# Performance work log

Measured on AMD Instinct MI355X. Metric: run time of the kernel, lower is better.

The kernel has to match this reference:

```python
import jax, jax.numpy as jnp
import numpy as np

N, E, T, F, HID, NCLS = 50000, 800000, 6, 64, 48, 2
LN_EPS = 1e-5


def setup_inputs() -> dict:
    key = jax.random.key(0)
    ks = jax.random.split(key, 24)
    p = lambda k, shape, s=0.1: jax.random.normal(k, shape, dtype=jnp.float32) * s
    inp = {
        "x_seq": jax.random.normal(ks[0], (T, N, F), dtype=jnp.float32),
        "edge_index": jax.random.randint(ks[1], (2, E), 0, N, dtype=jnp.int64),
        "edge_weight": jax.random.uniform(ks[2], (E,), dtype=jnp.float32),
        # GCN layer 0
        "W0": p(ks[3], (F, HID)), "b0": jnp.zeros((HID,), jnp.float32),
        "g0": jnp.ones((HID,), jnp.float32), "be0": jnp.zeros((HID,), jnp.float32),
        # GCN layer 1
        "W1": p(ks[4], (HID, HID)), "b1": jnp.zeros((HID,), jnp.float32),
        "g1": jnp.ones((HID,), jnp.float32), "be1": jnp.zeros((HID,), jnp.float32),
        # GRU (torch gate order: r, z, n)
        "W_ih": p(ks[5], (3 * HID, HID)), "W_hh": p(ks[6], (3 * HID, HID)),
        "b_ih": jnp.zeros((3 * HID,), jnp.float32), "b_hh": jnp.zeros((3 * HID,), jnp.float32),
        # classifier MLP
        "Wc1": p(ks[7], (HID, HID // 2)), "bc1": jnp.zeros((HID // 2,), jnp.float32),
        "Wc2": p(ks[8], (HID // 2, NCLS)), "bc2": jnp.zeros((NCLS,), jnp.float32),
    }
    return inp


def _layer_norm(x, g, b):
    mu = x.mean(-1, keepdims=True)
    var = ((x - mu) ** 2).mean(-1, keepdims=True)
    return (x - mu) * jax.lax.rsqrt(var + LN_EPS) * g + b


def reference(x_seq, edge_index, edge_weight, W0, b0, g0, be0, W1, b1, g1, be1,
              W_ih, W_hh, b_ih, b_hh, Wc1, bc1, Wc2, bc2):
    n = x_seq.shape[1]
    hid = W0.shape[1]
    row, col = edge_index[0], edge_index[1]
    # PyG GCNConv default: add self-loops (weight 1), symmetric normalization
    loop = jnp.arange(n)
    row_f = jnp.concatenate([row, loop])
    col_f = jnp.concatenate([col, loop])
    w_f = jnp.concatenate([edge_weight, jnp.ones((n,), edge_weight.dtype)])
    deg = jax.ops.segment_sum(w_f, col_f, num_segments=n)
    dis = jnp.where(deg > 0, jax.lax.rsqrt(jnp.maximum(deg, 1e-12)), 0.0)
    norm = dis[row_f] * w_f * dis[col_f]  # [E+N]

    def gcn(x, W, b):
        h = x @ W                              # [N, hid]
        msg = h[row_f] * norm[:, None]         # [E+N, hid]
        return jax.ops.segment_sum(msg, col_f, num_segments=n) + b

    def spatial(x_t):
        # layer 0: no residual (in_dim != hid)
        h1 = jax.nn.relu(_layer_norm(gcn(x_t, W0, b0), g0, be0))
        # layer 1: residual (dropout is eval-mode no-op)
        h2 = jax.nn.relu(_layer_norm(gcn(h1, W1, b1), g1, be1)) + h1
        return h2

    # sequential map over T keeps per-step [E,hid] message buffers small
    H = jax.lax.map(spatial, x_seq)            # [T, N, hid]

    def gru_step(h, x_t):
        gi = x_t @ W_ih.T + b_ih               # [N, 3*hid]
        gh = h @ W_hh.T + b_hh
        i_r, i_z, i_n = jnp.split(gi, 3, axis=-1)
        h_r, h_z, h_n = jnp.split(gh, 3, axis=-1)
        r = jax.nn.sigmoid(i_r + h_r)
        z = jax.nn.sigmoid(i_z + h_z)
        nv = jnp.tanh(i_n + r * h_n)
        h_new = (1.0 - z) * nv + z * h
        return h_new, None

    h0 = jnp.zeros((n, hid), x_seq.dtype)
    z_last, _ = jax.lax.scan(gru_step, h0, H)  # last hidden state [N, hid]

    logits = jax.nn.relu(z_last @ Wc1 + bc1) @ Wc2 + bc2  # [N, 2]
    return logits
```

## Files before the change

kernel.cpp:

```cpp
#include <hip/hip_runtime.h>
#include <hip/hip_fp16.h>
#include <math.h>

#define NN 50000
#define NE 800000
#define TT 6
#define HID 48
#define NB 196
#define LR 65

__device__ __forceinline__ float sigmoidf_(float x){ return 1.0f/(1.0f+__expf(-x)); }
__device__ __forceinline__ float tanhf_(float x){
  float xc = fminf(fmaxf(x,-15.f),15.f);
  float t = __expf(2.f*xc);
  return (t-1.f)/(t+1.f);
}
__device__ __forceinline__ unsigned f2bf(float x){
  unsigned u = __float_as_uint(x);
  return (u + 0x7fffu + ((u>>16)&1u)) >> 16;
}
__device__ __forceinline__ unsigned pack2(float a, float b){
  return f2bf(a) | (f2bf(b)<<16);
}
__device__ __forceinline__ float bflo(unsigned u){ return __uint_as_float(u<<16); }
__device__ __forceinline__ float bfhi(unsigned u){ return __uint_as_float(u & 0xffff0000u); }
__device__ __forceinline__ unsigned f2h(float x){
  return (unsigned)__half_as_ushort(__float2half(x));
}
__device__ __forceinline__ float h2f(unsigned u){
  return __half2float(__ushort_as_half((unsigned short)(u & 0xffffu)));
}
__device__ __forceinline__ unsigned pack2h(float a, float b){
  return f2h(a) | (f2h(b)<<16);
}

typedef __fp16 h2t __attribute__((ext_vector_type(2)));

__device__ __forceinline__ unsigned pkrtz(float a, float b){
#if __has_builtin(__builtin_amdgcn_cvt_pkrtz)
  auto r = __builtin_amdgcn_cvt_pkrtz(a, b);
  return __builtin_bit_cast(unsigned, r);
#else
  return pack2h(a, b);
#endif
}
__device__ __forceinline__ float dot2f(unsigned a, unsigned b, float c){
#if __has_builtin(__builtin_amdgcn_fdot2)
  return __builtin_amdgcn_fdot2(__builtin_bit_cast(h2t, a), __builtin_bit_cast(h2t, b), c, false);
#else
  h2t av = __builtin_bit_cast(h2t, a), bv = __builtin_bit_cast(h2t, b);
  return c + (float)av[0]*(float)bv[0] + (float)av[1]*(float)bv[1];
#endif
}

struct U3 { unsigned x,y,z; };

__device__ __forceinline__ int block_scan_incl(int x, int* wsum){
  int lane = threadIdx.x & 63, w = threadIdx.x >> 6;
  int v = x;
#pragma unroll
  for(int d=1; d<64; d<<=1){
    int u = __shfl_up(v, d, 64);
    if(lane >= d) v += u;
  }
  if(lane==63) wsum[w] = v;
  __syncthreads();
  int add = 0;
#pragma unroll
  for(int k=0;k<3;k++) if(w>k) add += wsum[k];
  return v + add;
}

__global__ __launch_bounds__(256) void k_setup(int* cnt,
                                               const float* __restrict__ Wih, const float* __restrict__ Whh,
                                               unsigned* Wxp, unsigned* Whp){
  int i = blockIdx.x*256+threadIdx.x;
  if(i<NN) cnt[i]=0;
  if(i < 24*144){
    int k2 = i/144, gf = i%144;
    Wxp[i] = pack2h(Wih[gf*48 + 2*k2], Wih[gf*48 + 2*k2 + 1]);
  }
  if(i < 6*24*24){
    int wv = i/576, r = i%576;
    int k2 = r/24, c = r%24;
    int row = (c<8) ? (wv*8 + c) : (c<16) ? (48 + wv*8 + c-8) : (96 + wv*8 + c-16);
    Whp[i] = pack2h(Whh[row*48 + 2*k2], Whh[row*48 + 2*k2 + 1]);
  }
}

__global__ __launch_bounds__(256) void k_cnt(const int* __restrict__ ei, int* cnt, int* pos){
  int e = blockIdx.x*256+threadIdx.x;
  if(e<NE){
    int c = ei[NE+e];
    pos[e] = atomicAdd(&cnt[c], 1);
  }
}

__global__ __launch_bounds__(256) void k_partA(const int* __restrict__ cnt, int* bsum){
  __shared__ int wsum[4];
  int i = blockIdx.x*256+threadIdx.x;
  int x = (i<NN)? cnt[i] : 0;
  int lane = threadIdx.x & 63, w = threadIdx.x >> 6;
  int v = x;
#pragma unroll
  for(int m=32;m>=1;m>>=1) v += __shfl_xor(v, m, 64);
  if(lane==0) wsum[w]=v;
  __syncthreads();
  if(threadIdx.x==0) bsum[blockIdx.x] = wsum[0]+wsum[1]+wsum[2]+wsum[3];
}

__global__ __launch_bounds__(256) void k_midB(const int* __restrict__ bsum, int* bpre, int* offs){
  __shared__ int wsum[4];
  int t = threadIdx.x;
  int x = (t<NB)? bsum[t] : 0;
  int incl = block_scan_incl(x, wsum);
  if(t<NB) bpre[t] = incl - x;
  if(t==255) offs[NN] = incl;
}

__global__ __launch_bounds__(256) void k_offsC(const int* __restrict__ cnt, const int* __restrict__ bpre,
                                               int* offs){
  __shared__ int wsum[4];
  int i = blockIdx.x*256+threadIdx.x;
  int x = (i<NN)? cnt[i] : 0;
  int incl = block_scan_incl(x, wsum);
  if(i<NN) offs[i] = bpre[blockIdx.x] + incl - x;
}

__global__ __launch_bounds__(256) void k_scatter(const int* __restrict__ ei, const float* __restrict__ ew,
                                                 const int* __restrict__ offs, const int* __restrict__ pos,
                                                 int2* __restrict__ csr){
  int e = blockIdx.x*256+threadIdx.x;
  if(e<NE){
    int c = ei[NE+e];
    int2 v; v.x = ei[e]; v.y = __float_as_int(ew[e]);
    csr[offs[c]+pos[e]] = v;
  }
}

__global__ __launch_bounds__(256) void k_deg(const int2* __restrict__ csr, const int* __restrict__ offs,
                                             float* dis){
  int i = blockIdx.x*256+threadIdx.x;
  if(i<NN){
    float s = 1.f;
    int e0=offs[i], e1=offs[i+1];
    for(int j=e0;j<e1;j++) s += __int_as_float(csr[j].y);
    dis[i] = rsqrtf(s);
  }
}

__global__ __launch_bounds__(256) void k_normE(int2* __restrict__ csr, const float* __restrict__ dis){
  int j = blockIdx.x*256+threadIdx.x;
  if(j<NE){
    int2 v = csr[j];
    v.y = __float_as_int(dis[v.x]*__int_as_float(v.y));
    csr[j] = v;
  }
}

__global__ __launch_bounds__(256) void k_mm0(const float* __restrict__ X, const float* __restrict__ W,
                                             unsigned* __restrict__ A){
  int s = __builtin_amdgcn_readfirstlane(threadIdx.x>>6);
  int n = blockIdx.x*64 + (threadIdx.x&63);
  if(n>=NN) return;
  const float* xb = X + (long long)n*64;
  const float* wb = W + 12*s;
  float acc[TT][12];
#pragma unroll
  for(int t=0;t<TT;t++)
#pragma unroll
    for(int j=0;j<12;j++) acc[t][j]=0.f;
#pragma unroll 2
  for(int k4=0;k4<16;k4++){
    float4 xv[TT];
#pragma unroll
    for(int t=0;t<TT;t++) xv[t] = *reinterpret_cast<const float4*>(xb + (long long)t*NN*64 + 4*k4);
#pragma unroll
    for(int q=0;q<4;q++){
      const float* wr = wb + (4*k4+q)*HID;
      float w[12];
#pragma unroll
      for(int j=0;j<12;j++) w[j]=wr[j];
#pragma unroll
      for(int t=0;t<TT;t++){
        float xs = (&xv[t].x)[q];
#pragma unroll
        for(int j=0;j<12;j++) acc[t][j] = fmaf(xs, w[j], acc[t][j]);
      }
    }
  }
  unsigned buf[36];
#pragma unroll
  for(int j=0;j<12;j++){
    buf[3*j  ]=pack2(acc[0][j],acc[1][j]);
    buf[3*j+1]=pack2(acc[2][j],acc[3][j]);
    buf[3*j+2]=pack2(acc[4][j],acc[5][j]);
  }
  uint4* o4 = reinterpret_cast<uint4*>(A + (long long)n*144 + 36*s);
#pragma unroll
  for(int q=0;q<9;q++) o4[q] = make_uint4(buf[4*q],buf[4*q+1],buf[4*q+2],buf[4*q+3]);
}

__global__ __launch_bounds__(256) void k_mm1(const float* __restrict__ X, const float* __restrict__ W,
                                             unsigned* __restrict__ A){
  int s = __builtin_amdgcn_readfirstlane(threadIdx.x>>6);
  int n = blockIdx.x*64 + (threadIdx.x&63);
  if(n>=NN) return;
  const float* xb = X + (long long)n*(TT*HID);
  const float* wb = W + 12*s;
  float acc[TT][12];
#pragma unroll
  for(int t=0;t<TT;t++)
#pragma unroll
    for(int j=0;j<12;j++) acc[t][j]=0.f;
#pragma unroll 2
  for(int k4=0;k4<12;k4++){
    float4 xv[TT];
#pragma unroll
    for(int t=0;t<TT;t++) xv[t] = *reinterpret_cast<const float4*>(xb + t*HID + 4*k4);
#pragma unroll
    for(int q=0;q<4;q++){
      const float* wr = wb + (4*k4+q)*HID;
      float w[12];
#pragma unroll
      for(int j=0;j<12;j++) w[j]=wr[j];
#pragma unroll
      for(int t=0;t<TT;t++){
        float xs = (&xv[t].x)[q];
#pragma unroll
        for(int j=0;j<12;j++) acc[t][j] = fmaf(xs, w[j], acc[t][j]);
      }
    }
  }
  unsigned buf[36];
#pragma unroll
  for(int j=0;j<12;j++){
    buf[3*j  ]=pack2(acc[0][j],acc[1][j]);
    buf[3*j+1]=pack2(acc[2][j],acc[3][j]);
    buf[3*j+2]=pack2(acc[4][j],acc[5][j]);
  }
  uint4* o4 = reinterpret_cast<uint4*>(A + (long long)n*144 + 36*s);
#pragma unroll
  for(int q=0;q<9;q++) o4[q] = make_uint4(buf[4*q],buf[4*q+1],buf[4*q+2],buf[4*q+3]);
}

__global__ __launch_bounds__(256) void k_agg(const unsigned* __restrict__ A, const float* __restrict__ bias,
                                             const float* __restrict__ gain, const float* __restrict__ beta,
                                             const float* __restrict__ resid, float* __restrict__ out,
                                             const int* __restrict__ offs, const int2* __restrict__ csr,
                                             const float* __restrict__ dis){
  int wid = (blockIdx.x*256+threadIdx.x)>>6;
  int lane = threadIdx.x & 63;
  if(wid>=NN) return;
  const bool act = lane<HID;
  const int f = act? lane : (HID-1);
  float dn = dis[wid];
  float acc[TT];
  {
    U3 v = *reinterpret_cast<const U3*>(A + (long long)wid*144 + 3*f);
    acc[0]=dn*bflo(v.x); acc[1]=dn*bfhi(v.x);
    acc[2]=dn*bflo(v.y); acc[3]=dn*bfhi(v.y);
    acc[4]=dn*bflo(v.z); acc[5]=dn*bfhi(v.z);
  }
  int e0=offs[wid], e1=offs[wid+1];
  int e=e0;
  for(; e+3<e1; e+=4){
    int2 i0=csr[e], i1=csr[e+1], i2=csr[e+2], i3=csr[e+3];
    U3 d0 = *reinterpret_cast<const U3*>(A + (long long)i0.x*144 + 3*f);
    U3 d1 = *reinterpret_cast<const U3*>(A + (long long)i1.x*144 + 3*f);
    U3 d2 = *reinterpret_cast<const U3*>(A + (long long)i2.x*144 + 3*f);
    U3 d3 = *reinterpret_cast<const U3*>(A + (long long)i3.x*144 + 3*f);
    float n0=__int_as_float(i0.y), n1=__int_as_float(i1.y);
    float n2=__int_as_float(i2.y), n3=__int_as_float(i3.y);
    acc[0]=fmaf(n0,bflo(d0.x),acc[0]); acc[1]=fmaf(n0,bfhi(d0.x),acc[1]);
    acc[2]=fmaf(n0,bflo(d0.y),acc[2]); acc[3]=fmaf(n0,bfhi(d0.y),acc[3]);
    acc[4]=fmaf(n0,bflo(d0.z),acc[4]); acc[5]=fmaf(n0,bfhi(d0.z),acc[5]);
    acc[0]=fmaf(n1,bflo(d1.x),acc[0]); acc[1]=fmaf(n1,bfhi(d1.x),acc[1]);
    acc[2]=fmaf(n1,bflo(d1.y),acc[2]); acc[3]=fmaf(n1,bfhi(d1.y),acc[3]);
    acc[4]=fmaf(n1,bflo(d1.z),acc[4]); acc[5]=fmaf(n1,bfhi(d1.z),acc[5]);
    acc[0]=fmaf(n2,bflo(d2.x),acc[0]); acc[1]=fmaf(n2,bfhi(d2.x),acc[1]);
    acc[2]=fmaf(n2,bflo(d2.y),acc[2]); acc[3]=fmaf(n2,bfhi(d2.y),acc[3]);
    acc[4]=fmaf(n2,bflo(d2.z),acc[4]); acc[5]=fmaf(n2,bfhi(d2.z),acc[5]);
    acc[0]=fmaf(n3,bflo(d3.x),acc[0]); acc[1]=fmaf(n3,bfhi(d3.x),acc[1]);
    acc[2]=fmaf(n3,bflo(d3.y),acc[2]); acc[3]=fmaf(n3,bfhi(d3.y),acc[3]);
    acc[4]=fmaf(n3,bflo(d3.z),acc[4]); acc[5]=fmaf(n3,bfhi(d3.z),acc[5]);
  }
  for(; e<e1; ++e){
    int2 i0=csr[e];
    U3 d0 = *reinterpret_cast<const U3*>(A + (long long)i0.x*144 + 3*f);
    float n0=__int_as_float(i0.y);
    acc[0]=fmaf(n0,bflo(d0.x),acc[0]); acc[1]=fmaf(n0,bfhi(d0.x),acc[1]);
    acc[2]=fmaf(n0,bflo(d0.y),acc[2]); acc[3]=fmaf(n0,bfhi(d0.y),acc[3]);
    acc[4]=fmaf(n0,bflo(d0.z),acc[4]); acc[5]=fmaf(n0,bfhi(d0.z),acc[5]);
  }
  float bb = bias[f], gg = gain[f], be = beta[f];
  const float rn = 1.0f/HID;
#pragma unroll
  for(int t=0;t<TT;t++){
    float val = fmaf(acc[t], dn, bb);
    float v = act? val : 0.f;
    float s = v, s2 = v*v;
#pragma unroll
    for(int m=32;m>=1;m>>=1){
      s  += __shfl_xor(s,  m, 64);
      s2 += __shfl_xor(s2, m, 64);
    }
    float mu  = s*rn;
    float var = fmaxf(s2*rn - mu*mu, 0.f);
    float y = (val-mu)*rsqrtf(var+1e-5f)*gg + be;
    y = fmaxf(y, 0.f);
    long long oidx = (long long)wid*(TT*HID) + t*HID + f;
    if(resid) y += resid[oidx];
    if(act) out[oidx] = y;
  }
}

__global__ __launch_bounds__(384) void k_gi(const float* __restrict__ X,
                                            const unsigned* __restrict__ Wxp,
                                            const float* __restrict__ bih,
                                            unsigned* __restrict__ gi){
  int wv = __builtin_amdgcn_readfirstlane(threadIdx.x>>6);
  int lane = threadIdx.x & 63;
  long long n = (long long)blockIdx.x*64 + lane;
  long long gn = (n < NN)? n : (NN-1);
  const bool wr = (n < NN);
  const float* xb = X + gn*(TT*HID) + wv*HID;
  unsigned xp[24];
#pragma unroll
  for(int q=0;q<12;q++){
    float4 v = *reinterpret_cast<const float4*>(xb + 4*q);
    xp[2*q]   = pkrtz(v.x, v.y);
    xp[2*q+1] = pkrtz(v.z, v.w);
  }
#pragma unroll 1
  for(int pass=0; pass<3; pass++){
    float acc[48];
#pragma unroll
    for(int j=0;j<48;j++) acc[j] = bih[pass*48+j];
#pragma unroll 2
    for(int k2=0;k2<24;k2++){
      unsigned xk = xp[k2];
#pragma unroll
      for(int c=0;c<2;c++){
        const unsigned* wp = Wxp + k2*144 + pass*48 + c*24;
        unsigned ws[24];
#pragma unroll
        for(int j=0;j<24;j++) ws[j]=wp[j];
#pragma unroll
        for(int j=0;j<24;j++) acc[c*24+j] = dot2f(xk, ws[j], acc[c*24+j]);
      }
    }
    if(wr){
      unsigned* ob = gi + ((long long)(wv*72 + pass*24))*NN + n;
#pragma unroll
      for(int m=0;m<24;m++){
        ob[(long long)m*NN] = pack2h(acc[2*m], acc[2*m+1]);
      }
    }
  }
}

__global__ __launch_bounds__(384) void k_gruH(const unsigned* __restrict__ gi,
                                              const unsigned* __restrict__ Whp,
                                              const float* __restrict__ bhh,
                                              const float* __restrict__ Wc1, const float* __restrict__ bc1,
                                              const float* __restrict__ Wc2, const float* __restrict__ bc2,
                                              float* __restrict__ out){
  __shared__ unsigned hb[2][24*64];
  int tid = threadIdx.x;
  int wv = __builtin_amdgcn_readfirstlane(tid>>6);
  int lane = tid & 63;
  int f0 = wv*8;
  long long n = (long long)blockIdx.x*64 + lane;
  long long gn = (n<NN)? n : (NN-1);

  for(int i=tid;i<24*64;i+=384) hb[0][i]=0u;

  float rb[8], zb[8], nb[8], hprev[8];
#pragma unroll
  for(int j=0;j<8;j++){
    rb[j]=bhh[f0+j]; zb[j]=bhh[48+f0+j]; nb[j]=bhh[96+f0+j];
    hprev[j]=0.f;
  }
  __syncthreads();

  int cur=0;
  for(int t=0;t<TT;t++){
    const unsigned* gb = gi + (long long)t*72*NN + gn;
    unsigned gpk[12];
#pragma unroll
    for(int m=0;m<4;m++){
      gpk[m]   = gb[(long long)(      wv*4+m)*NN];
      gpk[4+m] = gb[(long long)(24 +  wv*4+m)*NN];
      gpk[8+m] = gb[(long long)(48 +  wv*4+m)*NN];
    }
    float acc[24];
#pragma unroll
    for(int j=0;j<24;j++) acc[j]=0.f;
    const unsigned* hbc = &hb[cur][0];
#pragma unroll 2
    for(int k2=0;k2<24;k2++){
      const unsigned* wp = Whp + (wv*24+k2)*24;
      unsigned ws[24];
#pragma unroll
      for(int q=0;q<24;q++) ws[q]=wp[q];
      unsigned h2k = hbc[k2*64+lane];
#pragma unroll
      for(int c=0;c<24;c++) acc[c] = dot2f(h2k, ws[c], acc[c]);
    }
    unsigned* hw = &hb[cur^1][0];
    float hn[8];
#pragma unroll
    for(int j=0;j<8;j++){
      unsigned pr=gpk[j>>1], pz=gpk[4+(j>>1)], pn=gpk[8+(j>>1)];
      float gir = (j&1)? h2f(pr>>16) : h2f(pr);
      float giz = (j&1)? h2f(pz>>16) : h2f(pz);
      float gin = (j&1)? h2f(pn>>16) : h2f(pn);
      float r  = sigmoidf_(acc[j]+rb[j]+gir);
      float zg = sigmoidf_(acc[8+j]+zb[j]+giz);
      float ng = tanhf_(gin + r*(acc[16+j]+nb[j]));
      float hv = (1.f-zg)*ng + zg*hprev[j];
      hprev[j]=hv; hn[j]=hv;
    }
#pragma unroll
    for(int m=0;m<4;m++) hw[(wv*4+m)*64+lane] = pack2h(hn[2*m], hn[2*m+1]);
    __syncthreads();
    cur^=1;
  }

  if(wv==0 && n<NN){
    const unsigned* hbc=&hb[cur][0];
    float hv[24];
#pragma unroll
    for(int j=0;j<24;j++) hv[j]=bc1[j];
    for(int k2=0;k2<24;k2++){
      unsigned u = hbc[k2*64+lane];
      float hk0 = h2f(u), hk1 = h2f(u>>16);
      const float* w0 = Wc1 + (2*k2)*24;
      const float* w1 = Wc1 + (2*k2+1)*24;
#pragma unroll
      for(int j=0;j<24;j++) hv[j] = fmaf(hk0, w0[j], hv[j]);
#pragma unroll
      for(int j=0;j<24;j++) hv[j] = fmaf(hk1, w1[j], hv[j]);
    }
    float l0=bc2[0], l1=bc2[1];
#pragma unroll
    for(int j=0;j<24;j++){
      float a = fmaxf(hv[j],0.f);
      l0 = fmaf(a, Wc2[2*j],   l0);
      l1 = fmaf(a, Wc2[2*j+1], l1);
    }
    reinterpret_cast<float2*>(out)[n] = make_float2(l0,l1);
  }
}

static inline size_t al256(size_t x){ return (x+255)&~(size_t)255; }

extern "C" void kernel_launch(void* const* d_in, const int* in_sizes, int n_in,
                              void* d_out, int out_size, void* d_ws, size_t ws_size,
                              hipStream_t stream){
  const float* x_seq=(const float*)d_in[0];
  const int*   ei   =(const int*)d_in[1];
  const float* ew   =(const float*)d_in[2];
  const float* W0=(const float*)d_in[3];  const float* b0=(const float*)d_in[4];
  const float* g0=(const float*)d_in[5];  const float* be0=(const float*)d_in[6];
  const float* W1=(const float*)d_in[7];  const float* b1=(const float*)d_in[8];
  const float* g1=(const float*)d_in[9];  const float* be1=(const float*)d_in[10];
  const float* Wih=(const float*)d_in[11];const float* Whh=(const float*)d_in[12];
  const float* bih=(const float*)d_in[13];const float* bhh=(const float*)d_in[14];
  const float* Wc1=(const float*)d_in[15];const float* bc1=(const float*)d_in[16];
  const float* Wc2=(const float*)d_in[17];const float* bc2=(const float*)d_in[18];
  float* outp=(float*)d_out;

  char* p=(char*)d_ws; size_t off=0;
  auto alloc=[&](size_t bytes)->void*{ void* r=p+off; off=al256(off+bytes); return r; };
  float* dis    =(float*)alloc((size_t)NN*4);
  int*   cnt    =(int*)  alloc((size_t)NN*4);
  int*   offs   =(int*)  alloc((size_t)(NN+1)*4);
  int*   bsum   =(int*)  alloc((size_t)NB*4);
  int*   bpre   =(int*)  alloc((size_t)NB*4);
  int*   pos    =(int*)  alloc((size_t)NE*4);
  int2*  csr    =(int2*) alloc((size_t)NE*8);
  unsigned* Wxp =(unsigned*)alloc((size_t)24*144*4);
  unsigned* Whp =(unsigned*)alloc((size_t)6*24*24*4);
  unsigned* A   =(unsigned*)alloc((size_t)NN*576 + 1024);
  float* h1     =(float*)alloc((size_t)NN*TT*HID*4);
  float* h2     =(float*)alloc((size_t)NN*TT*HID*4);
  unsigned* gi  =(unsigned*)A;

  const int GN=(NN+255)/256, GE=(NE+255)/256;
  const int GMM=(NN+63)/64;
  const int GAGG=(NN*64+255)/256;
  const int GGRU=(NN+63)/64;

  k_setup  <<<GN,256,0,stream>>>(cnt,Wih,Whh,Wxp,Whp);
  k_cnt    <<<GE,256,0,stream>>>(ei,cnt,pos);
  k_partA  <<<NB,256,0,stream>>>(cnt,bsum);
  k_midB   <<<1,256,0,stream>>>(bsum,bpre,offs);
  k_offsC  <<<NB,256,0,stream>>>(cnt,bpre,offs);
  k_scatter<<<GE,256,0,stream>>>(ei,ew,offs,pos,csr);
  k_deg    <<<GN,256,0,stream>>>(csr,offs,dis);
  k_normE  <<<GE,256,0,stream>>>(csr,dis);

  k_mm0<<<GMM,256,0,stream>>>(x_seq, W0, A);
  k_agg<<<GAGG,256,0,stream>>>(A,b0,g0,be0,nullptr,h1,offs,csr,dis);
  k_mm1<<<GMM,256,0,stream>>>(h1, W1, A);
  k_agg<<<GAGG,256,0,stream>>>(A,b1,g1,be1,h1,h2,offs,csr,dis);
  k_gi  <<<GMM,384,0,stream>>>(h2, Wxp, bih, gi);
  k_gruH<<<GGRU,384,0,stream>>>(gi, Whp, bhh, Wc1,bc1,Wc2,bc2, outp);
}
```

Before: 699.6 us.

## Store GRU hidden state node-major in LDS and pad recurrent weight rows

The GRU kernel's shared hidden-state buffer becomes node-major with a padded stride of 28 words. Each lane now reads its whole 48-wide hidden vector with six 128-bit LDS loads into registers and writes its 8 outputs with one 128-bit store, instead of doing per-k scalar LDS reads. Recurrent weight rows are padded to 32 words so scalar loads are aligned, and the hidden bias is folded into the accumulator init. Loops in the input-projection and classifier kernels are fully unrolled, which adds register pressure.

```diff
diff --git a/kernel.cpp b/kernel.cpp
--- a/kernel.cpp
+++ b/kernel.cpp
@@ -7,7 +7,7 @@
 #define TT 6
 #define HID 48
 #define NB 196
-#define LR 65
+#define HS 28
 
 __device__ __forceinline__ float sigmoidf_(float x){ return 1.0f/(1.0f+__expf(-x)); }
 __device__ __forceinline__ float tanhf_(float x){
@@ -84,7 +84,7 @@
     int wv = i/576, r = i%576;
     int k2 = r/24, c = r%24;
     int row = (c<8) ? (wv*8 + c) : (c<16) ? (48 + wv*8 + c-8) : (96 + wv*8 + c-16);
-    Whp[i] = pack2h(Whh[row*48 + 2*k2], Whh[row*48 + 2*k2 + 1]);
+    Whp[(wv*24+k2)*32 + c] = pack2h(Whh[row*48 + 2*k2], Whh[row*48 + 2*k2 + 1]);
   }
 }
 
@@ -337,7 +337,7 @@
     float acc[48];
 #pragma unroll
     for(int j=0;j<48;j++) acc[j] = bih[pass*48+j];
-#pragma unroll 2
+#pragma unroll
     for(int k2=0;k2<24;k2++){
       unsigned xk = xp[k2];
 #pragma unroll
@@ -366,7 +366,7 @@
                                               const float* __restrict__ Wc1, const float* __restrict__ bc1,
                                               const float* __restrict__ Wc2, const float* __restrict__ bc2,
                                               float* __restrict__ out){
-  __shared__ unsigned hb[2][24*64];
+  __shared__ __align__(16) unsigned hb[2][64*HS];
   int tid = threadIdx.x;
   int wv = __builtin_amdgcn_readfirstlane(tid>>6);
   int lane = tid & 63;
@@ -374,7 +374,7 @@
   long long n = (long long)blockIdx.x*64 + lane;
   long long gn = (n<NN)? n : (NN-1);
 
-  for(int i=tid;i<24*64;i+=384) hb[0][i]=0u;
+  for(int i=tid;i<64*HS;i+=384) hb[0][i]=0u;
 
   float rb[8], zb[8], nb[8], hprev[8];
 #pragma unroll
@@ -394,21 +394,27 @@
       gpk[4+m] = gb[(long long)(24 +  wv*4+m)*NN];
       gpk[8+m] = gb[(long long)(48 +  wv*4+m)*NN];
     }
+    unsigned hreg[24];
+    {
+      const uint4* hr4 = reinterpret_cast<const uint4*>(&hb[cur][lane*HS]);
+#pragma unroll
+      for(int q=0;q<6;q++){
+        uint4 v = hr4[q];
+        hreg[4*q]=v.x; hreg[4*q+1]=v.y; hreg[4*q+2]=v.z; hreg[4*q+3]=v.w;
+      }
+    }
     float acc[24];
 #pragma unroll
-    for(int j=0;j<24;j++) acc[j]=0.f;
-    const unsigned* hbc = &hb[cur][0];
-#pragma unroll 2
+    for(int j=0;j<8;j++){ acc[j]=rb[j]; acc[8+j]=zb[j]; acc[16+j]=nb[j]; }
+#pragma unroll
     for(int k2=0;k2<24;k2++){
-      const unsigned* wp = Whp + (wv*24+k2)*24;
+      const unsigned* wp = Whp + (wv*24+k2)*32;
       unsigned ws[24];
 #pragma unroll
       for(int q=0;q<24;q++) ws[q]=wp[q];
-      unsigned h2k = hbc[k2*64+lane];
-#pragma unroll
-      for(int c=0;c<24;c++) acc[c] = dot2f(h2k, ws[c], acc[c]);
-    }
-    unsigned* hw = &hb[cur^1][0];
+#pragma unroll
+      for(int c=0;c<24;c++) acc[c] = dot2f(hreg[k2], ws[c], acc[c]);
+    }
     float hn[8];
 #pragma unroll
     for(int j=0;j<8;j++){
@@ -416,26 +422,35 @@
       float gir = (j&1)? h2f(pr>>16) : h2f(pr);
       float giz = (j&1)? h2f(pz>>16) : h2f(pz);
       float gin = (j&1)? h2f(pn>>16) : h2f(pn);
-      float r  = sigmoidf_(acc[j]+rb[j]+gir);
-      float zg = sigmoidf_(acc[8+j]+zb[j]+giz);
-      float ng = tanhf_(gin + r*(acc[16+j]+nb[j]));
+      float r  = sigmoidf_(acc[j]+gir);
+      float zg = sigmoidf_(acc[8+j]+giz);
+      float ng = tanhf_(gin + r*acc[16+j]);
       float hv = (1.f-zg)*ng + zg*hprev[j];
       hprev[j]=hv; hn[j]=hv;
     }
-#pragma unroll
-    for(int m=0;m<4;m++) hw[(wv*4+m)*64+lane] = pack2h(hn[2*m], hn[2*m+1]);
+    *reinterpret_cast<uint4*>(&hb[cur^1][lane*HS + wv*4]) =
+        make_uint4(pack2h(hn[0],hn[1]), pack2h(hn[2],hn[3]),
+                   pack2h(hn[4],hn[5]), pack2h(hn[6],hn[7]));
     __syncthreads();
     cur^=1;
   }
 
   if(wv==0 && n<NN){
-    const unsigned* hbc=&hb[cur][0];
+    unsigned hh[24];
+    {
+      const uint4* hr4 = reinterpret_cast<const uint4*>(&hb[cur][lane*HS]);
+#pragma unroll
+      for(int q=0;q<6;q++){
+        uint4 v = hr4[q];
+        hh[4*q]=v.x; hh[4*q+1]=v.y; hh[4*q+2]=v.z; hh[4*q+3]=v.w;
+      }
+    }
     float hv[24];
 #pragma unroll
     for(int j=0;j<24;j++) hv[j]=bc1[j];
+#pragma unroll
     for(int k2=0;k2<24;k2++){
-      unsigned u = hbc[k2*64+lane];
-      float hk0 = h2f(u), hk1 = h2f(u>>16);
+      float hk0 = h2f(hh[k2]), hk1 = h2f(hh[k2]>>16);
       const float* w0 = Wc1 + (2*k2)*24;
       const float* w1 = Wc1 + (2*k2+1)*24;
 #pragma unroll
@@ -482,7 +497,7 @@
   int*   pos    =(int*)  alloc((size_t)NE*4);
   int2*  csr    =(int2*) alloc((size_t)NE*8);
   unsigned* Wxp =(unsigned*)alloc((size_t)24*144*4);
-  unsigned* Whp =(unsigned*)alloc((size_t)6*24*24*4);
+  unsigned* Whp =(unsigned*)alloc((size_t)6*24*32*4);
   unsigned* A   =(unsigned*)alloc((size_t)NN*576 + 1024);
   float* h1     =(float*)alloc((size_t)NN*TT*HID*4);
   float* h2     =(float*)alloc((size_t)NN*TT*HID*4);
```

Measured after the change: 923.5 us. +32.0%, slower.

## Fuse GRU input projection into recurrent kernel, staging inputs in LDS

Applied to the files above, without the earlier changes.

Removes the separate k_gi kernel, which wrote fp16 gate pre-activations for all timesteps to global memory, and computes the input projection inside the recurrent GRU kernel. Each block stages its nodes' six timesteps of h2 into shared memory as packed fp16, then each timestep does combined dot2 accumulation over the hidden and input weights from one interleaved weight array. Input and hidden biases are folded into the accumulator initialisation. This drops a large global write and re-read of the gi buffer and one launch, at the cost of more shared memory per block (about 49KB) and more registers in the recurrent loop, which may lower occupancy.

```diff
diff --git a/kernel.cpp b/kernel.cpp
--- a/kernel.cpp
+++ b/kernel.cpp
@@ -7,7 +7,6 @@
 #define TT 6
 #define HID 48
 #define NB 196
-#define LR 65
 
 __device__ __forceinline__ float sigmoidf_(float x){ return 1.0f/(1.0f+__expf(-x)); }
 __device__ __forceinline__ float tanhf_(float x){
@@ -73,18 +72,16 @@
 
 __global__ __launch_bounds__(256) void k_setup(int* cnt,
                                                const float* __restrict__ Wih, const float* __restrict__ Whh,
-                                               unsigned* Wxp, unsigned* Whp){
+                                               unsigned* Wall){
   int i = blockIdx.x*256+threadIdx.x;
   if(i<NN) cnt[i]=0;
-  if(i < 24*144){
-    int k2 = i/144, gf = i%144;
-    Wxp[i] = pack2h(Wih[gf*48 + 2*k2], Wih[gf*48 + 2*k2 + 1]);
-  }
-  if(i < 6*24*24){
-    int wv = i/576, r = i%576;
-    int k2 = r/24, c = r%24;
-    int row = (c<8) ? (wv*8 + c) : (c<16) ? (48 + wv*8 + c-8) : (96 + wv*8 + c-16);
-    Whp[i] = pack2h(Whh[row*48 + 2*k2], Whh[row*48 + 2*k2 + 1]);
+  if(i < 6*24*48){
+    int wv = i/1152, r = i%1152;
+    int k2 = r/48, c = r%48;
+    int cc = (c<24)? c : (c-24);
+    int row = (cc<8) ? (wv*8 + cc) : (cc<16) ? (48 + wv*8 + cc-8) : (96 + wv*8 + cc-16);
+    const float* Wsrc = (c<24)? Whh : Wih;
+    Wall[i] = pack2h(Wsrc[row*48 + 2*k2], Wsrc[row*48 + 2*k2 + 1]);
   }
 }
 
@@ -315,57 +312,13 @@
   }
 }
 
-__global__ __launch_bounds__(384) void k_gi(const float* __restrict__ X,
-                                            const unsigned* __restrict__ Wxp,
-                                            const float* __restrict__ bih,
-                                            unsigned* __restrict__ gi){
-  int wv = __builtin_amdgcn_readfirstlane(threadIdx.x>>6);
-  int lane = threadIdx.x & 63;
-  long long n = (long long)blockIdx.x*64 + lane;
-  long long gn = (n < NN)? n : (NN-1);
-  const bool wr = (n < NN);
-  const float* xb = X + gn*(TT*HID) + wv*HID;
-  unsigned xp[24];
-#pragma unroll
-  for(int q=0;q<12;q++){
-    float4 v = *reinterpret_cast<const float4*>(xb + 4*q);
-    xp[2*q]   = pkrtz(v.x, v.y);
-    xp[2*q+1] = pkrtz(v.z, v.w);
-  }
-#pragma unroll 1
-  for(int pass=0; pass<3; pass++){
-    float acc[48];
-#pragma unroll
-    for(int j=0;j<48;j++) acc[j] = bih[pass*48+j];
-#pragma unroll 2
-    for(int k2=0;k2<24;k2++){
-      unsigned xk = xp[k2];
-#pragma unroll
-      for(int c=0;c<2;c++){
-        const unsigned* wp = Wxp + k2*144 + pass*48 + c*24;
-        unsigned ws[24];
-#pragma unroll
-        for(int j=0;j<24;j++) ws[j]=wp[j];
-#pragma unroll
-        for(int j=0;j<24;j++) acc[c*24+j] = dot2f(xk, ws[j], acc[c*24+j]);
-      }
-    }
-    if(wr){
-      unsigned* ob = gi + ((long long)(wv*72 + pass*24))*NN + n;
-#pragma unroll
-      for(int m=0;m<24;m++){
-        ob[(long long)m*NN] = pack2h(acc[2*m], acc[2*m+1]);
-      }
-    }
-  }
-}
-
-__global__ __launch_bounds__(384) void k_gruH(const unsigned* __restrict__ gi,
-                                              const unsigned* __restrict__ Whp,
-                                              const float* __restrict__ bhh,
-                                              const float* __restrict__ Wc1, const float* __restrict__ bc1,
-                                              const float* __restrict__ Wc2, const float* __restrict__ bc2,
-                                              float* __restrict__ out){
+__global__ __launch_bounds__(384) void k_gruF2(const float* __restrict__ X,
+                                               const unsigned* __restrict__ Wall,
+                                               const float* __restrict__ bih, const float* __restrict__ bhh,
+                                               const float* __restrict__ Wc1, const float* __restrict__ bc1,
+                                               const float* __restrict__ Wc2, const float* __restrict__ bc2,
+                                               float* __restrict__ out){
+  __shared__ unsigned xall[TT*24*64];
   __shared__ unsigned hb[2][24*64];
   int tid = threadIdx.x;
   int wv = __builtin_amdgcn_readfirstlane(tid>>6);
@@ -374,51 +327,57 @@
   long long n = (long long)blockIdx.x*64 + lane;
   long long gn = (n<NN)? n : (NN-1);
 
+  {
+    const float* xb = X + gn*(TT*HID) + wv*HID;
+#pragma unroll
+    for(int q=0;q<12;q++){
+      float4 v = *reinterpret_cast<const float4*>(xb + 4*q);
+      xall[(wv*24 + 2*q  )*64 + lane] = pkrtz(v.x, v.y);
+      xall[(wv*24 + 2*q+1)*64 + lane] = pkrtz(v.z, v.w);
+    }
+  }
   for(int i=tid;i<24*64;i+=384) hb[0][i]=0u;
 
-  float rb[8], zb[8], nb[8], hprev[8];
+  float rb[8], zb[8], nbi[8], nbh[8], hprev[8];
 #pragma unroll
   for(int j=0;j<8;j++){
-    rb[j]=bhh[f0+j]; zb[j]=bhh[48+f0+j]; nb[j]=bhh[96+f0+j];
+    rb[j] = bih[f0+j]    + bhh[f0+j];
+    zb[j] = bih[48+f0+j] + bhh[48+f0+j];
+    nbi[j]= bih[96+f0+j];
+    nbh[j]= bhh[96+f0+j];
     hprev[j]=0.f;
   }
   __syncthreads();
 
   int cur=0;
   for(int t=0;t<TT;t++){
-    const unsigned* gb = gi + (long long)t*72*NN + gn;
-    unsigned gpk[12];
-#pragma unroll
-    for(int m=0;m<4;m++){
-      gpk[m]   = gb[(long long)(      wv*4+m)*NN];
-      gpk[4+m] = gb[(long long)(24 +  wv*4+m)*NN];
-      gpk[8+m] = gb[(long long)(48 +  wv*4+m)*NN];
-    }
-    float acc[24];
-#pragma unroll
-    for(int j=0;j<24;j++) acc[j]=0.f;
+    float acc[24], accn[8];
+#pragma unroll
+    for(int j=0;j<8;j++){ acc[j]=rb[j]; acc[8+j]=zb[j]; acc[16+j]=nbh[j]; accn[j]=nbi[j]; }
     const unsigned* hbc = &hb[cur][0];
+    const unsigned* xtc = &xall[t*24*64];
 #pragma unroll 2
     for(int k2=0;k2<24;k2++){
-      const unsigned* wp = Whp + (wv*24+k2)*24;
-      unsigned ws[24];
-#pragma unroll
-      for(int q=0;q<24;q++) ws[q]=wp[q];
+      const unsigned* wp = Wall + (wv*24+k2)*48;
+      unsigned ws[48];
+#pragma unroll
+      for(int q=0;q<48;q++) ws[q]=wp[q];
       unsigned h2k = hbc[k2*64+lane];
-#pragma unroll
-      for(int c=0;c<24;c++) acc[c] = dot2f(h2k, ws[c], acc[c]);
+      unsigned xk  = xtc[k2*64+lane];
+#pragma unroll
+      for(int c=0;c<24;c++) acc[c]  = dot2f(h2k, ws[c],    acc[c]);
+#pragma unroll
+      for(int c=0;c<16;c++) acc[c]  = dot2f(xk,  ws[24+c], acc[c]);
+#pragma unroll
+      for(int c=0;c<8;c++)  accn[c] = dot2f(xk,  ws[40+c], accn[c]);
     }
     unsigned* hw = &hb[cur^1][0];
     float hn[8];
 #pragma unroll
     for(int j=0;j<8;j++){
-      unsigned pr=gpk[j>>1], pz=gpk[4+(j>>1)], pn=gpk[8+(j>>1)];
-      float gir = (j&1)? h2f(pr>>16) : h2f(pr);
-      float giz = (j&1)? h2f(pz>>16) : h2f(pz);
-      float gin = (j&1)? h2f(pn>>16) : h2f(pn);
-      float r  = sigmoidf_(acc[j]+rb[j]+gir);
-      float zg = sigmoidf_(acc[8+j]+zb[j]+giz);
-      float ng = tanhf_(gin + r*(acc[16+j]+nb[j]));
+      float r  = sigmoidf_(acc[j]);
+      float zg = sigmoidf_(acc[8+j]);
+      float ng = tanhf_(accn[j] + r*acc[16+j]);
       float hv = (1.f-zg)*ng + zg*hprev[j];
       hprev[j]=hv; hn[j]=hv;
     }
@@ -433,6 +392,7 @@
     float hv[24];
 #pragma unroll
     for(int j=0;j<24;j++) hv[j]=bc1[j];
+#pragma unroll 2
     for(int k2=0;k2<24;k2++){
       unsigned u = hbc[k2*64+lane];
       float hk0 = h2f(u), hk1 = h2f(u>>16);
@@ -481,19 +441,17 @@
   int*   bpre   =(int*)  alloc((size_t)NB*4);
   int*   pos    =(int*)  alloc((size_t)NE*4);
   int2*  csr    =(int2*) alloc((size_t)NE*8);
-  unsigned* Wxp =(unsigned*)alloc((size_t)24*144*4);
-  unsigned* Whp =(unsigned*)alloc((size_t)6*24*24*4);
+  unsigned* Wall=(unsigned*)alloc((size_t)6*24*48*4);
   unsigned* A   =(unsigned*)alloc((size_t)NN*576 + 1024);
   float* h1     =(float*)alloc((size_t)NN*TT*HID*4);
   float* h2     =(float*)alloc((size_t)NN*TT*HID*4);
-  unsigned* gi  =(unsigned*)A;
 
   const int GN=(NN+255)/256, GE=(NE+255)/256;
   const int GMM=(NN+63)/64;
   const int GAGG=(NN*64+255)/256;
   const int GGRU=(NN+63)/64;
 
-  k_setup  <<<GN,256,0,stream>>>(cnt,Wih,Whh,Wxp,Whp);
+  k_setup  <<<GN,256,0,stream>>>(cnt,Wih,Whh,Wall);
   k_cnt    <<<GE,256,0,stream>>>(ei,cnt,pos);
   k_partA  <<<NB,256,0,stream>>>(cnt,bsum);
   k_midB   <<<1,256,0,stream>>>(bsum,bpre,offs);
@@ -506,6 +464,5 @@
   k_agg<<<GAGG,256,0,stream>>>(A,b0,g0,be0,nullptr,h1,offs,csr,dis);
   k_mm1<<<GMM,256,0,stream>>>(h1, W1, A);
   k_agg<<<GAGG,256,0,stream>>>(A,b1,g1,be1,h1,h2,offs,csr,dis);
-  k_gi  <<<GMM,384,0,stream>>>(h2, Wxp, bih, gi);
-  k_gruH<<<GGRU,384,0,stream>>>(gi, Whp, bhh, Wc1,bc1,Wc2,bc2, outp);
-}
+  k_gruF2<<<GGRU,384,0,stream>>>(h2, Wall, bih,bhh, Wc1,bc1,Wc2,bc2, outp);
+}
```

Result: no change. 694.5 us (-0.7%).
